# Performance work log

Hardware: AMD Instinct MI355X
Metric: run time of the kernel (lower is better)

The kernel has to match this reference:

```python
import jax, jax.numpy as jnp
import numpy as np

ALPHA = 100.0
EPS = 1e-12  # torch F.normalize eps


def setup_inputs() -> dict:
    key = jax.random.key(0)
    k1, k2 = jax.random.split(key)
    N, C, H, W, K = 32, 512, 56, 56, 64
    x = jax.random.normal(k1, (N, C, H, W), dtype=jnp.float32)
    centroids = jax.random.uniform(k2, (K, C), dtype=jnp.float32)  # torch.rand
    # _init_params: conv weight/bias are independent params initialized from centroids
    conv_w = 2.0 * ALPHA * centroids                      # (K, C), 1x1 conv kernel
    conv_b = -ALPHA * jnp.linalg.norm(centroids, axis=1)  # (K,)
    return {"x": x, "centroids": centroids, "conv_w": conv_w, "conv_b": conv_b}


def reference(x, centroids, conv_w, conv_b):
    N, C, H, W = x.shape
    K = centroids.shape[0]
    P = H * W
    xf = x.reshape(N, C, P)  # local descriptors, (N, C, P)

    # 1x1 conv == per-pixel linear; softmax over clusters
    logits = jnp.einsum('ncp,kc->nkp', xf, conv_w) + conv_b[None, :, None]
    a = jax.nn.softmax(logits, axis=1)  # (N, K, P)

    # Faithful to original: centroids.view(C, K) is a row-major RESHAPE, not transpose
    cent_r = jnp.reshape(centroids, (C, K))  # (C, K)

    # Algebraic rewrite of sum_p a[n,k,p] * (x[n,c,p] - cent_r[c,k]):
    # avoids the (N, C, K, P) intermediate entirely.
    vlad = jnp.einsum('ncp,nkp->nck', xf, a) - cent_r[None] * a.sum(-1)[:, None, :]  # (N, C, K)

    # intra-normalization over dim=2 (clusters), as in original code
    vlad = vlad / jnp.clip(jnp.linalg.norm(vlad, axis=2, keepdims=True), EPS)
    vlad = vlad.reshape(N, C * K)
    vlad = vlad / jnp.clip(jnp.linalg.norm(vlad, axis=1, keepdims=True), EPS)
    return vlad
```

## Files before the change

kernel.cpp:

```cpp
#include <hip/hip_runtime.h>
#include <math.h>

#define N_DIM 32
#define C_DIM 512
#define K_DIM 64
#define P_DIM 3136
#define ABLK 49


__global__ __launch_bounds__(256) void k_prep(const float* __restrict__ conv_w,
                                              float* __restrict__ wt) {
    const int b = blockIdx.x, t = threadIdx.x;
#pragma unroll
    for (int r = 0; r < 4; ++r) {
        int idx = b * 1024 + r * 256 + t;
        int c = idx >> 6, k = idx & 63;
        wt[idx] = conv_w[k * C_DIM + c];
    }
}

__global__ __launch_bounds__(64, 2) void k_logits(const float* __restrict__ x,
                                                  const float* __restrict__ wt,
                                                  const float* __restrict__ bias,
                                                  float* __restrict__ a_t,
                                                  float* __restrict__ asum_part) {
    __shared__ float xs[2][16][64];
    __shared__ float wsh[2][16][64];
    const int lane = threadIdx.x;
    const int n    = blockIdx.y;
    const int pblk = blockIdx.x;
    const int p0   = pblk * 64;
    const int kg   = lane & 7;
    const int pxg  = lane >> 3;

    float acc[8][8];
    {
        float4 b0 = *(const float4*)(bias + kg * 8);
        float4 b1 = *(const float4*)(bias + kg * 8 + 4);
        float br[8] = {b0.x, b0.y, b0.z, b0.w, b1.x, b1.y, b1.z, b1.w};
#pragma unroll
        for (int i = 0; i < 8; ++i)
#pragma unroll
            for (int j = 0; j < 8; ++j) acc[i][j] = br[j];
    }

    const float* xb = x + (size_t)n * C_DIM * P_DIM + p0;

    float4 xv[4], wv[4];
#define STAGE_LOAD(c0_) do {                                                      \
    _Pragma("unroll")                                                             \
    for (int i_ = 0; i_ < 4; ++i_) {                                              \
        int f_ = lane + 64 * i_;                                                  \
        xv[i_] = *(const float4*)(xb + (size_t)((c0_) + (f_ >> 4)) * P_DIM        \
                                     + (f_ & 15) * 4);                            \
        wv[i_] = *(const float4*)(wt + (size_t)(c0_) * K_DIM + f_ * 4);           \
    } } while (0)
#define STAGE_WRITE(buf_) do {                                                    \
    _Pragma("unroll")                                                             \
    for (int i_ = 0; i_ < 4; ++i_) {                                              \
        int f_ = lane + 64 * i_;                                                  \
        *(float4*)&xs[buf_][f_ >> 4][(f_ & 15) * 4]  = xv[i_];                    \
        *(float4*)&wsh[buf_][f_ >> 4][(f_ & 15) * 4] = wv[i_];                    \
    } } while (0)

    STAGE_LOAD(0);
    STAGE_WRITE(0);
    STAGE_LOAD(16);

    for (int cc = 0; cc < C_DIM; cc += 16) {
        const int buf = (cc >> 4) & 1;
        if (cc + 16 < C_DIM) {
            STAGE_WRITE(buf ^ 1);
            if (cc + 32 < C_DIM) STAGE_LOAD(cc + 32);
        }
#pragma unroll
        for (int c = 0; c < 16; ++c) {
            float4 x0 = *(const float4*)&xs[buf][c][pxg * 8];
            float4 x1 = *(const float4*)&xs[buf][c][pxg * 8 + 4];
            float4 w0 = *(const float4*)&wsh[buf][c][kg * 8];
            float4 w1 = *(const float4*)&wsh[buf][c][kg * 8 + 4];
            float xr[8] = {x0.x, x0.y, x0.z, x0.w, x1.x, x1.y, x1.z, x1.w};
            float wr[8] = {w0.x, w0.y, w0.z, w0.w, w1.x, w1.y, w1.z, w1.w};
#pragma unroll
            for (int i = 0; i < 8; ++i)
#pragma unroll
                for (int j = 0; j < 8; ++j)
                    acc[i][j] = fmaf(xr[i], wr[j], acc[i][j]);
        }
    }
#undef STAGE_LOAD
#undef STAGE_WRITE

    float sk[8] = {0.f, 0.f, 0.f, 0.f, 0.f, 0.f, 0.f, 0.f};
#pragma unroll
    for (int i = 0; i < 8; ++i) {
        float m = acc[i][0];
#pragma unroll
        for (int j = 1; j < 8; ++j) m = fmaxf(m, acc[i][j]);
        m = fmaxf(m, __shfl_xor(m, 1));
        m = fmaxf(m, __shfl_xor(m, 2));
        m = fmaxf(m, __shfl_xor(m, 4));
        float e[8], s = 0.f;
#pragma unroll
        for (int j = 0; j < 8; ++j) { e[j] = __expf(acc[i][j] - m); s += e[j]; }
        s += __shfl_xor(s, 1);
        s += __shfl_xor(s, 2);
        s += __shfl_xor(s, 4);
        const float inv = 1.0f / s;
        float4 o0, o1;
        o0.x = e[0] * inv; o0.y = e[1] * inv; o0.z = e[2] * inv; o0.w = e[3] * inv;
        o1.x = e[4] * inv; o1.y = e[5] * inv; o1.z = e[6] * inv; o1.w = e[7] * inv;
        float* ap = a_t + ((size_t)n * P_DIM + p0 + pxg * 8 + i) * K_DIM + kg * 8;
        *(float4*)ap = o0;
        *(float4*)(ap + 4) = o1;
        sk[0] += o0.x; sk[1] += o0.y; sk[2] += o0.z; sk[3] += o0.w;
        sk[4] += o1.x; sk[5] += o1.y; sk[6] += o1.z; sk[7] += o1.w;
    }
#pragma unroll
    for (int j = 0; j < 8; ++j) {
        sk[j] += __shfl_xor(sk[j], 8);
        sk[j] += __shfl_xor(sk[j], 16);
        sk[j] += __shfl_xor(sk[j], 32);
    }
    if (pxg == 0) {
        float* pp = asum_part + ((size_t)n * ABLK + pblk) * K_DIM + kg * 8;
        float4 s0, s1;
        s0.x = sk[0]; s0.y = sk[1]; s0.z = sk[2]; s0.w = sk[3];
        s1.x = sk[4]; s1.y = sk[5]; s1.z = sk[6]; s1.w = sk[7];
        *(float4*)pp = s0;
        *(float4*)(pp + 4) = s1;
    }
}

__global__ __launch_bounds__(256) void k_red(const float* __restrict__ asum_part,
                                             float* __restrict__ asum) {
    const int idx = blockIdx.x * 256 + threadIdx.x;
    const int n = idx >> 6, k = idx & 63;
    float s = 0.f;
#pragma unroll
    for (int b = 0; b < ABLK; ++b)
        s += asum_part[((size_t)n * ABLK + b) * K_DIM + k];
    asum[idx] = s;
}

__global__ __launch_bounds__(128) void k_gemm2(const float* __restrict__ x,
                                               const float* __restrict__ a_t,
                                               float* __restrict__ part,
                                               int pslice) {
    __shared__ float xs[16][132];
    __shared__ float as[16][64];
    const int tid = threadIdx.x;
    const int c0 = blockIdx.x * 128;
    const int n  = blockIdx.y;
    const int s  = blockIdx.z;
    const int p0 = s * pslice;
    const int tc = tid >> 3;
    const int tk = tid & 7;

    float acc[8][8];
#pragma unroll
    for (int i = 0; i < 8; ++i)
#pragma unroll
        for (int j = 0; j < 8; ++j) acc[i][j] = 0.f;

    const float* xb = x + ((size_t)n * C_DIM + c0) * P_DIM + p0;
    const float* ab = a_t + ((size_t)n * P_DIM + p0) * K_DIM;

    float4 xv[4], av[2];
#pragma unroll
    for (int i = 0; i < 4; ++i) {
        int f = tid + 128 * i;
        xv[i] = *(const float4*)(xb + (size_t)(f >> 2) * P_DIM + (f & 3) * 4);
    }
#pragma unroll
    for (int i = 0; i < 2; ++i) {
        int f = tid + 128 * i;
        av[i] = *(const float4*)(ab + (size_t)(f >> 4) * K_DIM + (f & 15) * 4);
    }

    for (int pb = 0; pb < pslice; pb += 16) {
        __syncthreads();
#pragma unroll
        for (int i = 0; i < 4; ++i) {
            int f = tid + 128 * i;
            int c = f >> 2, pe = (f & 3) * 4;
            xs[pe + 0][c] = xv[i].x;
            xs[pe + 1][c] = xv[i].y;
            xs[pe + 2][c] = xv[i].z;
            xs[pe + 3][c] = xv[i].w;
        }
#pragma unroll
        for (int i = 0; i < 2; ++i) {
            int f = tid + 128 * i;
            *(float4*)&as[f >> 4][(f & 15) * 4] = av[i];
        }
        __syncthreads();

        if (pb + 16 < pslice) {
            const float* xc = xb + pb + 16;
            const float* ac = ab + (size_t)(pb + 16) * K_DIM;
#pragma unroll
            for (int i = 0; i < 4; ++i) {
                int f = tid + 128 * i;
                xv[i] = *(const float4*)(xc + (size_t)(f >> 2) * P_DIM + (f & 3) * 4);
            }
#pragma unroll
            for (int i = 0; i < 2; ++i) {
                int f = tid + 128 * i;
                av[i] = *(const float4*)(ac + (size_t)(f >> 4) * K_DIM + (f & 15) * 4);
            }
        }

#pragma unroll 4
        for (int p = 0; p < 16; ++p) {
            float4 x0 = *(const float4*)&xs[p][tc * 8];
            float4 x1 = *(const float4*)&xs[p][tc * 8 + 4];
            float4 a0 = *(const float4*)&as[p][tk * 8];
            float4 a1 = *(const float4*)&as[p][tk * 8 + 4];
            float xr[8] = {x0.x, x0.y, x0.z, x0.w, x1.x, x1.y, x1.z, x1.w};
            float ar[8] = {a0.x, a0.y, a0.z, a0.w, a1.x, a1.y, a1.z, a1.w};
#pragma unroll
            for (int i = 0; i < 8; ++i)
#pragma unroll
                for (int j = 0; j < 8; ++j)
                    acc[i][j] = fmaf(xr[i], ar[j], acc[i][j]);
        }
    }

    float* po = part + (((size_t)s * N_DIM + n) * C_DIM + c0 + tc * 8) * K_DIM + tk * 8;
#pragma unroll
    for (int i = 0; i < 8; ++i) {
        float4 o0, o1;
        o0.x = acc[i][0]; o0.y = acc[i][1]; o0.z = acc[i][2]; o0.w = acc[i][3];
        o1.x = acc[i][4]; o1.y = acc[i][5]; o1.z = acc[i][6]; o1.w = acc[i][7];
        *(float4*)&po[(size_t)i * K_DIM] = o0;
        *(float4*)&po[(size_t)i * K_DIM + 4] = o1;
    }
}

template <int S>
__global__ __launch_bounds__(256) void k_intra(const float* __restrict__ part,
                                               const float* __restrict__ cent,
                                               const float* __restrict__ asum,
                                               float* __restrict__ out,
                                               float* __restrict__ ssb) {
    const int w = (blockIdx.x * 256 + threadIdx.x) >> 6;
    const int lane = threadIdx.x & 63;
    const int n = w >> 9;
    const int c = w & 511;
    const size_t off = ((size_t)n * C_DIM + c) * K_DIM + lane;
    const size_t stride = (size_t)N_DIM * C_DIM * K_DIM;

    float v = 0.f;
#pragma unroll
    for (int s = 0; s < S; ++s) v += part[s * stride + off];
    v -= cent[c * K_DIM + lane] * asum[n * K_DIM + lane];

    float ss = v * v;
#pragma unroll
    for (int o = 32; o > 0; o >>= 1) ss += __shfl_xor(ss, o);

    const float denom = fmaxf(sqrtf(ss), 1e-12f);
    out[off] = v / denom;
    if (lane == 0) ssb[w] = ss / (denom * denom);
}

__global__ __launch_bounds__(256) void k_gsum(const float* __restrict__ ssb,
                                              float* __restrict__ gsum) {
    const int n = blockIdx.x, t = threadIdx.x;
    float s = ssb[n * C_DIM + t] + ssb[n * C_DIM + t + 256];
    __shared__ float red[256];
    red[t] = s;
    __syncthreads();
    for (int o = 128; o > 0; o >>= 1) {
        if (t < o) red[t] += red[t + o];
        __syncthreads();
    }
    if (t == 0) gsum[n] = red[0];
}

__global__ __launch_bounds__(256) void k_final(float* __restrict__ out,
                                               const float* __restrict__ gsum) {
    const size_t i = (size_t)blockIdx.x * 256 + threadIdx.x;
    const int n = (int)(i >> 15);
    const float g = sqrtf(gsum[n]);
    out[i] = out[i] / fmaxf(g, 1e-12f);
}

extern "C" void kernel_launch(void* const* d_in, const int* in_sizes, int n_in,
                              void* d_out, int out_size, void* d_ws, size_t ws_size,
                              hipStream_t stream) {
    const float* x      = (const float*)d_in[0];
    const float* cent   = (const float*)d_in[1];
    const float* conv_w = (const float*)d_in[2];
    const float* conv_b = (const float*)d_in[3];

    float* ws    = (float*)d_ws;
    float* wt    = ws;
    float* a_t   = wt + 32768;
    float* asum  = a_t + (size_t)N_DIM * P_DIM * K_DIM;
    float* apart = asum + 2048;
    float* gsum  = apart + (size_t)N_DIM * ABLK * K_DIM;
    float* ssb   = gsum + 32;
    float* part  = ssb + 16384;
    float* out   = (float*)d_out;

    const size_t base_f = (size_t)(part - ws);
    const size_t cxk = (size_t)N_DIM * C_DIM * K_DIM;
    int S = 14;
    if (ws_size < (base_f + 14 * cxk) * 4) S = 7;
    if (ws_size < (base_f + 7 * cxk) * 4) S = 2;
    const int pslice = P_DIM / S;

    hipLaunchKernelGGL(k_prep,   dim3(32),        dim3(256), 0, stream, conv_w, wt);
    hipLaunchKernelGGL(k_logits, dim3(ABLK, 32),  dim3(64),  0, stream, x, wt, conv_b, a_t, apart);
    hipLaunchKernelGGL(k_red,    dim3(8),         dim3(256), 0, stream, apart, asum);
    hipLaunchKernelGGL(k_gemm2,  dim3(4, 32, S),  dim3(128), 0, stream, x, a_t, part, pslice);
    if (S == 14)
        hipLaunchKernelGGL(k_intra<14>, dim3(4096), dim3(256), 0, stream, part, cent, asum, out, ssb);
    else if (S == 7)
        hipLaunchKernelGGL(k_intra<7>,  dim3(4096), dim3(256), 0, stream, part, cent, asum, out, ssb);
    else
        hipLaunchKernelGGL(k_intra<2>,  dim3(4096), dim3(256), 0, stream, part, cent, asum, out, ssb);
    hipLaunchKernelGGL(k_gsum,   dim3(32),        dim3(256), 0, stream, ssb, gsum);
    hipLaunchKernelGGL(k_final,  dim3(4096),      dim3(256), 0, stream, out, gsum);
}
```

Baseline: 519.8 us.

## Use direct global-to-LDS async loads with manual waitcnt pipelining in logits GEMM

Replaces the register-staged global loads plus LDS stores in the logits kernel with global_load_lds builtins that write straight into shared memory. The main loop becomes a two-buffer pipeline controlled by explicit s_waitcnt vmcnt/lgkmcnt so the next chunk is fetched while the current one is computed. The aim is to cut VGPR pressure and the LDS write instructions. The risk is that the hand-written waitcnt ordering is subtle and may be unsafe, since the block is a single wave with no barrier.

```diff
diff --git a/kernel.cpp b/kernel.cpp
--- a/kernel.cpp
+++ b/kernel.cpp
@@ -19,13 +19,19 @@
     }
 }
 
+__device__ __forceinline__ void gld_lds16(const float* g, void* l) {
+    __builtin_amdgcn_global_load_lds(
+        (const __attribute__((address_space(1))) void*)g,
+        (__attribute__((address_space(3))) void*)l, 16, 0, 0);
+}
+
 __global__ __launch_bounds__(64, 2) void k_logits(const float* __restrict__ x,
                                                   const float* __restrict__ wt,
                                                   const float* __restrict__ bias,
                                                   float* __restrict__ a_t,
                                                   float* __restrict__ asum_part) {
-    __shared__ float xs[2][16][64];
-    __shared__ float wsh[2][16][64];
+    __shared__ __align__(16) float xs[2][16][64];
+    __shared__ __align__(16) float wsh[2][16][64];
     const int lane = threadIdx.x;
     const int n    = blockIdx.y;
     const int pblk = blockIdx.x;
@@ -46,50 +52,45 @@
 
     const float* xb = x + (size_t)n * C_DIM * P_DIM + p0;
 
-    float4 xv[4], wv[4];
-#define STAGE_LOAD(c0_) do {                                                      \
+#define STAGE(chk_, buf_) do {                                                    \
+    const int c0_ = (chk_) * 16;                                                  \
     _Pragma("unroll")                                                             \
     for (int i_ = 0; i_ < 4; ++i_) {                                              \
         int f_ = lane + 64 * i_;                                                  \
-        xv[i_] = *(const float4*)(xb + (size_t)((c0_) + (f_ >> 4)) * P_DIM        \
-                                     + (f_ & 15) * 4);                            \
-        wv[i_] = *(const float4*)(wt + (size_t)(c0_) * K_DIM + f_ * 4);           \
+        gld_lds16(xb + (size_t)(c0_ + (f_ >> 4)) * P_DIM + (f_ & 15) * 4,         \
+                  (char*)&xs[buf_][0][0] + i_ * 1024);                            \
+        gld_lds16(wt + (size_t)c0_ * K_DIM + f_ * 4,                              \
+                  (char*)&wsh[buf_][0][0] + i_ * 1024);                           \
     } } while (0)
-#define STAGE_WRITE(buf_) do {                                                    \
+
+#define COMPUTE(buf_) do {                                                        \
     _Pragma("unroll")                                                             \
-    for (int i_ = 0; i_ < 4; ++i_) {                                              \
-        int f_ = lane + 64 * i_;                                                  \
-        *(float4*)&xs[buf_][f_ >> 4][(f_ & 15) * 4]  = xv[i_];                    \
-        *(float4*)&wsh[buf_][f_ >> 4][(f_ & 15) * 4] = wv[i_];                    \
+    for (int c_ = 0; c_ < 16; ++c_) {                                             \
+        float4 x0 = *(const float4*)&xs[buf_][c_][pxg * 8];                       \
+        float4 x1 = *(const float4*)&xs[buf_][c_][pxg * 8 + 4];                   \
+        float4 w0 = *(const float4*)&wsh[buf_][c_][kg * 8];                       \
+        float4 w1 = *(const float4*)&wsh[buf_][c_][kg * 8 + 4];                   \
+        float xr[8] = {x0.x, x0.y, x0.z, x0.w, x1.x, x1.y, x1.z, x1.w};           \
+        float wr[8] = {w0.x, w0.y, w0.z, w0.w, w1.x, w1.y, w1.z, w1.w};           \
+        _Pragma("unroll")                                                         \
+        for (int i_ = 0; i_ < 8; ++i_)                                            \
+            _Pragma("unroll")                                                     \
+            for (int j_ = 0; j_ < 8; ++j_)                                        \
+                acc[i_][j_] = fmaf(xr[i_], wr[j_], acc[i_][j_]);                  \
     } } while (0)
 
-    STAGE_LOAD(0);
-    STAGE_WRITE(0);
-    STAGE_LOAD(16);
-
-    for (int cc = 0; cc < C_DIM; cc += 16) {
-        const int buf = (cc >> 4) & 1;
-        if (cc + 16 < C_DIM) {
-            STAGE_WRITE(buf ^ 1);
-            if (cc + 32 < C_DIM) STAGE_LOAD(cc + 32);
-        }
-#pragma unroll
-        for (int c = 0; c < 16; ++c) {
-            float4 x0 = *(const float4*)&xs[buf][c][pxg * 8];
-            float4 x1 = *(const float4*)&xs[buf][c][pxg * 8 + 4];
-            float4 w0 = *(const float4*)&wsh[buf][c][kg * 8];
-            float4 w1 = *(const float4*)&wsh[buf][c][kg * 8 + 4];
-            float xr[8] = {x0.x, x0.y, x0.z, x0.w, x1.x, x1.y, x1.z, x1.w};
-            float wr[8] = {w0.x, w0.y, w0.z, w0.w, w1.x, w1.y, w1.z, w1.w};
-#pragma unroll
-            for (int i = 0; i < 8; ++i)
-#pragma unroll
-                for (int j = 0; j < 8; ++j)
-                    acc[i][j] = fmaf(xr[i], wr[j], acc[i][j]);
-        }
-    }
-#undef STAGE_LOAD
-#undef STAGE_WRITE
+    STAGE(0, 0);
+    STAGE(1, 1);
+    for (int i = 0; i < 31; ++i) {
+        asm volatile("s_waitcnt vmcnt(8)" ::: "memory");
+        if (i & 1) COMPUTE(1); else COMPUTE(0);
+        asm volatile("s_waitcnt lgkmcnt(0)" ::: "memory");
+        if (i < 30) STAGE(i + 2, i & 1);
+    }
+    asm volatile("s_waitcnt vmcnt(0)" ::: "memory");
+    COMPUTE(1);
+#undef STAGE
+#undef COMPUTE
 
     float sk[8] = {0.f, 0.f, 0.f, 0.f, 0.f, 0.f, 0.f, 0.f};
 #pragma unroll
```

New measurement: 503.7 us. 3.1% less time.
